# Performance work log

Measured on AMD Instinct MI355X. Metric: run time of the kernel, lower is better.

Reference implementation:

```python
import jax, jax.numpy as jnp
import numpy as np

NBINS = (128, 64, 32)
N_REGIONS = 5000
N_REGIONS_OI = 500
N_POINTS = 262144
SUM_H = sum(NBINS)            # 224
SUM_W = sum(n - 1 for n in NBINS)  # 221


def _spline_level(x, uw_region, uh_pt, local_ix):
    """One quadratic-spline level.
    x: [N] inputs in [0,1); uw_region: [R, n-1] region unnormalized widths;
    uh_pt: [N, n] per-point unnormalized heights (embedding + delta);
    local_ix: [N] int mapping points -> rows of uw_region.
    """
    # region-level widths / bin locations (calculate_widths / calculate_bin_locations)
    widths = jax.nn.softmax(uw_region, axis=-1)                # [R, n-1]
    bl = jnp.cumsum(widths, axis=-1)
    bl = bl.at[:, -1].set(1.0)
    bin_locations = jnp.pad(bl, ((0, 0), (1, 0)))              # [R, n]

    # gather per point (index_select(0, local_region_ix))
    widths_pt = widths[local_ix]                               # [N, n-1]
    bin_loc_pt = bin_locations[local_ix]                       # [N, n]

    # calculate_heights: exp then normalize so trapezoid integral == 1
    he = jnp.exp(uh_pt)                                        # [N, n]
    area = jnp.sum(0.5 * (he[:, :-1] + he[:, 1:]) * widths_pt, axis=-1, keepdims=True)
    heights = he / area                                        # [N, n]

    # calculate_bin_left_cdf
    cdf = jnp.cumsum(0.5 * (heights[:, :-1] + heights[:, 1:]) * widths_pt, axis=-1)
    cdf = cdf.at[:, -1].set(1.0)
    bin_left_cdf = jnp.pad(cdf, ((0, 0), (1, 0)))              # [N, n]

    # searchsorted(bin_locations, x, side='left') - 1, clamped to valid bins
    n = bin_loc_pt.shape[-1]
    bin_idx = jnp.clip(jnp.sum(bin_loc_pt < x[:, None], axis=-1) - 1, 0, n - 2)  # [N]

    take = lambda a, i: jnp.take_along_axis(a, i[:, None], axis=-1)[:, 0]
    in_loc = take(bin_loc_pt, bin_idx)
    in_w = take(widths_pt, bin_idx)
    in_cdf = take(bin_left_cdf, bin_idx)
    h_l = take(heights, bin_idx)
    h_r = take(heights, bin_idx + 1)

    alpha = (x - in_loc) / in_w
    a = 0.5 * (h_r - h_l) * in_w
    b = h_l * in_w
    out = a * alpha * alpha + b * alpha + in_cdf
    logabsdet = jnp.log(alpha * (h_r - h_l) + h_l)
    return out, logabsdet


def setup_inputs() -> dict:
    key = jax.random.key(0)
    k1, k2, k3, k4, k5, k6 = jax.random.split(key, 6)
    x = jax.random.uniform(k1, (N_POINTS,), dtype=jnp.float32)
    regions_oi = jax.random.randint(k2, (N_REGIONS_OI,), 0, N_REGIONS, dtype=jnp.int32)
    local_region_ix = jax.random.randint(k3, (N_POINTS,), 0, N_REGIONS_OI, dtype=jnp.int32)
    delta = jax.random.normal(k4, (N_POINTS, SUM_H), dtype=jnp.float32)
    # learned sparse embedding tables (init to random for a nontrivial baseline)
    heights_emb = 0.1 * jax.random.normal(k5, (N_REGIONS, SUM_H), dtype=jnp.float32)
    widths_emb = 0.1 * jax.random.normal(k6, (N_REGIONS, SUM_W), dtype=jnp.float32)
    return {"x": x, "regions_oi": regions_oi, "local_region_ix": local_region_ix,
            "delta": delta, "heights_emb": heights_emb, "widths_emb": widths_emb}


def reference(x, regions_oi, local_region_ix, delta, heights_emb, widths_emb):
    uh_all = heights_emb[regions_oi]   # [R, 224]
    uw_all = widths_emb[regions_oi]    # [R, 221]
    out = x
    logdet = jnp.zeros_like(x)
    oh = 0
    ow = 0
    for n in NBINS:
        uw = uw_all[:, ow:ow + (n - 1)]                               # [R, n-1]
        uh_pt = uh_all[local_region_ix][:, oh:oh + n] + delta[:, oh:oh + n]  # [N, n]
        out, ld = _spline_level(out, uw, uh_pt, local_region_ix)
        logdet = logdet + ld
        oh += n
        ow += n - 1
    return out, logdet
```

## Files before the change

kernel.cpp:

```cpp
#include <hip/hip_runtime.h>

#define NPOINTS 262144
#define SUMH 224
#define SUMW 221
#define NREG 500

__device__ __forceinline__ float rlane(float v, int l) {
  return __int_as_float(__builtin_amdgcn_readlane(__float_as_int(v), l));
}
template<int CTRL>
__device__ __forceinline__ float dpp_add(float x) {
  return x + __int_as_float(__builtin_amdgcn_update_dpp(0, __float_as_int(x), CTRL, 0xF, 0xF, false));
}
template<int CTRL>
__device__ __forceinline__ float dpp_max(float x) {
  return fmaxf(x, __int_as_float(__builtin_amdgcn_update_dpp(__float_as_int(x), __float_as_int(x), CTRL, 0xF, 0xF, false)));
}
__device__ __forceinline__ float wave_sum(float x) {
  x = dpp_add<0x111>(x); x = dpp_add<0x112>(x); x = dpp_add<0x114>(x);
  x = dpp_add<0x118>(x); x = dpp_add<0x142>(x); x = dpp_add<0x143>(x);
  return rlane(x, 63);
}
__device__ __forceinline__ float wave_max(float x) {
  x = dpp_max<0x111>(x); x = dpp_max<0x112>(x); x = dpp_max<0x114>(x);
  x = dpp_max<0x118>(x); x = dpp_max<0x142>(x); x = dpp_max<0x143>(x);
  return rlane(x, 63);
}

__device__ __forceinline__ float grp_sum(float x) {
  x += __int_as_float(__builtin_amdgcn_update_dpp(0, __float_as_int(x), 0xB1,  0xF, 0xF, true));
  x += __int_as_float(__builtin_amdgcn_update_dpp(0, __float_as_int(x), 0x4E,  0xF, 0xF, true));
  x += __int_as_float(__builtin_amdgcn_update_dpp(0, __float_as_int(x), 0x141, 0xF, 0xF, true));
  x += __int_as_float(__builtin_amdgcn_update_dpp(0, __float_as_int(x), 0x140, 0xF, 0xF, true));
  return x;
}
__device__ __forceinline__ int grp_sum_i(int x) {
  x += __builtin_amdgcn_update_dpp(0, x, 0xB1,  0xF, 0xF, true);
  x += __builtin_amdgcn_update_dpp(0, x, 0x4E,  0xF, 0xF, true);
  x += __builtin_amdgcn_update_dpp(0, x, 0x141, 0xF, 0xF, true);
  x += __builtin_amdgcn_update_dpp(0, x, 0x140, 0xF, 0xF, true);
  return x;
}


template<int M, int SRC, int DST, int NB>
__device__ __forceinline__ void region_level(const float* __restrict__ wrow,
    float* __restrict__ BL, float* __restrict__ HW, float* __restrict__ HM,
    int lane, float* lds)
{
  float v0 = (lane < M) ? wrow[SRC + lane] : -1e30f;
  float v1 = -1e30f;
  if constexpr (NB == 128) { if (lane + 64 < M) v1 = wrow[SRC + lane + 64]; }
  float m = wave_max(fmaxf(v0, v1));
  float e0 = __expf(v0 - m);
  float e1 = (NB == 128) ? __expf(v1 - m) : 0.0f;
  float s = wave_sum(e0 + e1);
  float inv = 1.0f / s;
  if (lane < NB) lds[lane] = e0;
  if constexpr (NB == 128) lds[lane + 64] = e1;
  __syncthreads();
  if (lane < NB) {
    HW[DST + lane] = 0.5f * e0 * inv;
    HM[DST + lane] = (lane == 0) ? 0.0f : 0.5f * lds[lane - 1] * inv;
  }
  if constexpr (NB == 128) {
    HW[DST + lane + 64] = 0.5f * e1 * inv;
    HM[DST + lane + 64] = 0.5f * lds[lane + 63] * inv;
  }
  if (lane == 0) {
    BL[DST] = 0.0f;
    float run = 0.0f;
    for (int k = 0; k < M; ++k) {
      run += lds[k];
      BL[DST + 1 + k] = (k == M - 1) ? 1.0f : run * inv;
    }
  }
  __syncthreads();
}

__global__ void __launch_bounds__(64) region_kernel(
    const int* __restrict__ roi, const float* __restrict__ wemb,
    float* __restrict__ wsBL, float* __restrict__ wsHW, float* __restrict__ wsHM)
{
  __shared__ float lds[128];
  int rix = blockIdx.x;
  int lane = threadIdx.x;
  int greg = roi[rix];
  const float* wrow = wemb + (size_t)greg * SUMW;
  float* BL = wsBL + (size_t)rix * SUMH;
  float* HW = wsHW + (size_t)rix * SUMH;
  float* HM = wsHM + (size_t)rix * SUMH;
  region_level<127,   0,   0, 128>(wrow, BL, HW, HM, lane, lds);
  region_level< 63, 127, 128,  64>(wrow, BL, HW, HM, lane, lds);
  region_level< 31, 190, 192,  32>(wrow, BL, HW, HM, lane, lds);
}


template<int NB, int OFF, int C>
__device__ __forceinline__ void level(float& xv, float& logdet,
    const float* __restrict__ U, const float* __restrict__ D,
    const float* __restrict__ BLt, const float* __restrict__ HWt,
    const float* __restrict__ HMt, int s)
{
  float u[C], d[C], bl[C], hw[C], hm[C];
  if constexpr (C >= 4) {
#pragma unroll
    for (int v = 0; v < C / 4; ++v) {
      int c0 = OFF + (s * (C / 4) + v) * 4;
      float4 a = *(const float4*)(U   + c0);
      float4 b = *(const float4*)(D   + c0);
      float4 e = *(const float4*)(BLt + c0);
      float4 f = *(const float4*)(HWt + c0);
      float4 g = *(const float4*)(HMt + c0);
      u[4*v+0]=a.x; u[4*v+1]=a.y; u[4*v+2]=a.z; u[4*v+3]=a.w;
      d[4*v+0]=b.x; d[4*v+1]=b.y; d[4*v+2]=b.z; d[4*v+3]=b.w;
      bl[4*v+0]=e.x; bl[4*v+1]=e.y; bl[4*v+2]=e.z; bl[4*v+3]=e.w;
      hw[4*v+0]=f.x; hw[4*v+1]=f.y; hw[4*v+2]=f.z; hw[4*v+3]=f.w;
      hm[4*v+0]=g.x; hm[4*v+1]=g.y; hm[4*v+2]=g.z; hm[4*v+3]=g.w;
    }
  } else {
    int c0 = OFF + s * 2;
    float2 a = *(const float2*)(U   + c0);
    float2 b = *(const float2*)(D   + c0);
    float2 e = *(const float2*)(BLt + c0);
    float2 f = *(const float2*)(HWt + c0);
    float2 g = *(const float2*)(HMt + c0);
    u[0]=a.x; u[1]=a.y; d[0]=b.x; d[1]=b.y; bl[0]=e.x; bl[1]=e.y;
    hw[0]=f.x; hw[1]=f.y; hm[0]=g.x; hm[1]=g.y;
  }

  int cnt = 0;
  float he[C];
#pragma unroll
  for (int i = 0; i < C; ++i) {
    he[i] = __expf(u[i] + d[i]);
    cnt += (bl[i] < xv) ? 1 : 0;
  }
  cnt = grp_sum_i(cnt);
  int bi = min(max(cnt - 1, 0), NB - 2);

  float area = 0.0f, pr = 0.0f;
#pragma unroll
  for (int i = 0; i < C; ++i) {
    float t = he[i] * (hw[i] + hm[i]);
    area += t;
    int j = s * C + i;
    pr += (j <= bi) ? t : 0.0f;
  }
  area = grp_sum(area);
  pr   = grp_sum(pr);

  float inloc = BLt[OFF + bi];
  float hwbi  = HWt[OFF + bi];
  float hl = __expf(U[OFF + bi]     + D[OFF + bi]);
  float hr = __expf(U[OFF + bi + 1] + D[OFF + bi + 1]);

  float part = pr - hl * hwbi;
  float inw = 2.0f * hwbi;
  float inv_area = __builtin_amdgcn_rcpf(area);
  float alpha = (xv - inloc) * __builtin_amdgcn_rcpf(inw);
  float dh = hr - hl;
  float outv = ((0.5f * dh * alpha + hl) * alpha * inw + part) * inv_area;
  logdet += (__log2f(alpha * dh + hl) - __log2f(area)) * 0.69314718055994531f;
  xv = outv;
}

__global__ void __launch_bounds__(256) spline_kernel(
    const float* __restrict__ x, const int* __restrict__ roi,
    const int* __restrict__ lix, const float* __restrict__ delta,
    const float* __restrict__ hemb,
    const float* __restrict__ wsBL, const float* __restrict__ wsHW,
    const float* __restrict__ wsHM, float* __restrict__ out)
{
  int tid  = (int)(blockIdx.x * blockDim.x + threadIdx.x);
  int wid  = tid >> 6;
  int lane = (int)(threadIdx.x & 63);
  int grp  = lane >> 4;
  int s    = lane & 15;
  int pid  = wid * 4 + grp;
  if (pid >= NPOINTS) return;

  float xv = x[pid];
  int r    = lix[pid];
  int greg = roi[r];
  const float* U   = hemb  + (size_t)greg * SUMH;
  const float* D   = delta + (size_t)pid  * SUMH;
  const float* BLt = wsBL  + (size_t)r    * SUMH;
  const float* HWt = wsHW  + (size_t)r    * SUMH;
  const float* HMt = wsHM  + (size_t)r    * SUMH;

  float logdet = 0.0f;
  level<128,   0, 8>(xv, logdet, U, D, BLt, HWt, HMt, s);
  level< 64, 128, 4>(xv, logdet, U, D, BLt, HWt, HMt, s);
  level< 32, 192, 2>(xv, logdet, U, D, BLt, HWt, HMt, s);

  if (s == 0) {
    out[pid] = xv;
    out[NPOINTS + pid] = logdet;
  }
}


extern "C" void kernel_launch(void* const* d_in, const int* in_sizes, int n_in,
                              void* d_out, int out_size, void* d_ws, size_t ws_size,
                              hipStream_t stream) {
  const float* x     = (const float*)d_in[0];
  const int*   roi   = (const int*)  d_in[1];
  const int*   lix   = (const int*)  d_in[2];
  const float* delta = (const float*)d_in[3];
  const float* hemb  = (const float*)d_in[4];
  const float* wemb  = (const float*)d_in[5];

  float* wsBL = (float*)d_ws;
  float* wsHW = wsBL + (size_t)NREG * SUMH;
  float* wsHM = wsHW + (size_t)NREG * SUMH;

  region_kernel<<<NREG, 64, 0, stream>>>(roi, wemb, wsBL, wsHW, wsHM);
  spline_kernel<<<NPOINTS / 16, 256, 0, stream>>>(x, roi, lix, delta, hemb,
                                                  wsBL, wsHW, wsHM, (float*)d_out);
}
```

Before: 389.0 us.

## Precompute per-level prefix sums and fetch bin values via lane permutes

Splits each spline level into an x-independent prep phase (load, exp, prefix scan of trapezoid areas, log/reciprocal of area) and an x-dependent apply phase. All three levels' loads and scans are issued up front, so memory latency overlaps instead of being serialized by the x dependency chain. The scattered global re-reads of the selected bin's values are replaced with register selects plus ds_bpermute across the 16-lane group. This costs more live registers (three levels' arrays held at once), which may reduce occupancy. The early-return bounds check is also removed.

```diff
diff --git a/kernel.cpp b/kernel.cpp
--- a/kernel.cpp
+++ b/kernel.cpp
@@ -40,6 +40,23 @@
   x += __builtin_amdgcn_update_dpp(0, x, 0x141, 0xF, 0xF, true);
   x += __builtin_amdgcn_update_dpp(0, x, 0x140, 0xF, 0xF, true);
   return x;
+}
+__device__ __forceinline__ float row_scan_incl(float x) {
+  x += __int_as_float(__builtin_amdgcn_update_dpp(0, __float_as_int(x), 0x111, 0xF, 0xF, true));
+  x += __int_as_float(__builtin_amdgcn_update_dpp(0, __float_as_int(x), 0x112, 0xF, 0xF, true));
+  x += __int_as_float(__builtin_amdgcn_update_dpp(0, __float_as_int(x), 0x114, 0xF, 0xF, true));
+  x += __int_as_float(__builtin_amdgcn_update_dpp(0, __float_as_int(x), 0x118, 0xF, 0xF, true));
+  return x;
+}
+__device__ __forceinline__ float bperm(int lane, float v) {
+  return __int_as_float(__builtin_amdgcn_ds_bpermute(lane << 2, __float_as_int(v)));
+}
+template<int C>
+__device__ __forceinline__ float sel(const float (&a)[C], int idx) {
+  float r = a[0];
+#pragma unroll
+  for (int i = 1; i < C; ++i) r = (idx == i) ? a[i] : r;
+  return r;
 }
 
 
@@ -96,74 +113,84 @@
 }
 
 
-template<int NB, int OFF, int C>
-__device__ __forceinline__ void level(float& xv, float& logdet,
-    const float* __restrict__ U, const float* __restrict__ D,
-    const float* __restrict__ BLt, const float* __restrict__ HWt,
-    const float* __restrict__ HMt, int s)
-{
-  float u[C], d[C], bl[C], hw[C], hm[C];
-  if constexpr (C >= 4) {
-#pragma unroll
-    for (int v = 0; v < C / 4; ++v) {
-      int c0 = OFF + (s * (C / 4) + v) * 4;
-      float4 a = *(const float4*)(U   + c0);
-      float4 b = *(const float4*)(D   + c0);
-      float4 e = *(const float4*)(BLt + c0);
-      float4 f = *(const float4*)(HWt + c0);
-      float4 g = *(const float4*)(HMt + c0);
-      u[4*v+0]=a.x; u[4*v+1]=a.y; u[4*v+2]=a.z; u[4*v+3]=a.w;
-      d[4*v+0]=b.x; d[4*v+1]=b.y; d[4*v+2]=b.z; d[4*v+3]=b.w;
-      bl[4*v+0]=e.x; bl[4*v+1]=e.y; bl[4*v+2]=e.z; bl[4*v+3]=e.w;
-      hw[4*v+0]=f.x; hw[4*v+1]=f.y; hw[4*v+2]=f.z; hw[4*v+3]=f.w;
-      hm[4*v+0]=g.x; hm[4*v+1]=g.y; hm[4*v+2]=g.z; hm[4*v+3]=g.w;
+template<int NB, int OFF, int C, int LOG2C>
+struct Level {
+  float he[C], bl[C], hw[C], Q[C];
+  float larea, invarea;
+
+  __device__ __forceinline__ void prep(const float* __restrict__ U,
+      const float* __restrict__ D, const float* __restrict__ BLt,
+      const float* __restrict__ HWt, const float* __restrict__ HMt, int s)
+  {
+    float t[C];
+    if constexpr (C >= 4) {
+#pragma unroll
+      for (int v = 0; v < C / 4; ++v) {
+        int c0 = OFF + (s * (C / 4) + v) * 4;
+        float4 a = *(const float4*)(U   + c0);
+        float4 b = *(const float4*)(D   + c0);
+        float4 e = *(const float4*)(BLt + c0);
+        float4 f = *(const float4*)(HWt + c0);
+        float4 g = *(const float4*)(HMt + c0);
+        he[4*v+0] = __expf(a.x + b.x); he[4*v+1] = __expf(a.y + b.y);
+        he[4*v+2] = __expf(a.z + b.z); he[4*v+3] = __expf(a.w + b.w);
+        bl[4*v+0]=e.x; bl[4*v+1]=e.y; bl[4*v+2]=e.z; bl[4*v+3]=e.w;
+        hw[4*v+0]=f.x; hw[4*v+1]=f.y; hw[4*v+2]=f.z; hw[4*v+3]=f.w;
+        t[4*v+0] = he[4*v+0]*(f.x+g.x); t[4*v+1] = he[4*v+1]*(f.y+g.y);
+        t[4*v+2] = he[4*v+2]*(f.z+g.z); t[4*v+3] = he[4*v+3]*(f.w+g.w);
+      }
+    } else {
+      int c0 = OFF + s * 2;
+      float2 a = *(const float2*)(U   + c0);
+      float2 b = *(const float2*)(D   + c0);
+      float2 e = *(const float2*)(BLt + c0);
+      float2 f = *(const float2*)(HWt + c0);
+      float2 g = *(const float2*)(HMt + c0);
+      he[0] = __expf(a.x + b.x); he[1] = __expf(a.y + b.y);
+      bl[0]=e.x; bl[1]=e.y; hw[0]=f.x; hw[1]=f.y;
+      t[0] = he[0]*(f.x+g.x); t[1] = he[1]*(f.y+g.y);
     }
-  } else {
-    int c0 = OFF + s * 2;
-    float2 a = *(const float2*)(U   + c0);
-    float2 b = *(const float2*)(D   + c0);
-    float2 e = *(const float2*)(BLt + c0);
-    float2 f = *(const float2*)(HWt + c0);
-    float2 g = *(const float2*)(HMt + c0);
-    u[0]=a.x; u[1]=a.y; d[0]=b.x; d[1]=b.y; bl[0]=e.x; bl[1]=e.y;
-    hw[0]=f.x; hw[1]=f.y; hm[0]=g.x; hm[1]=g.y;
-  }
-
-  int cnt = 0;
-  float he[C];
-#pragma unroll
-  for (int i = 0; i < C; ++i) {
-    he[i] = __expf(u[i] + d[i]);
-    cnt += (bl[i] < xv) ? 1 : 0;
-  }
-  cnt = grp_sum_i(cnt);
-  int bi = min(max(cnt - 1, 0), NB - 2);
-
-  float area = 0.0f, pr = 0.0f;
-#pragma unroll
-  for (int i = 0; i < C; ++i) {
-    float t = he[i] * (hw[i] + hm[i]);
-    area += t;
-    int j = s * C + i;
-    pr += (j <= bi) ? t : 0.0f;
-  }
-  area = grp_sum(area);
-  pr   = grp_sum(pr);
-
-  float inloc = BLt[OFF + bi];
-  float hwbi  = HWt[OFF + bi];
-  float hl = __expf(U[OFF + bi]     + D[OFF + bi]);
-  float hr = __expf(U[OFF + bi + 1] + D[OFF + bi + 1]);
-
-  float part = pr - hl * hwbi;
-  float inw = 2.0f * hwbi;
-  float inv_area = __builtin_amdgcn_rcpf(area);
-  float alpha = (xv - inloc) * __builtin_amdgcn_rcpf(inw);
-  float dh = hr - hl;
-  float outv = ((0.5f * dh * alpha + hl) * alpha * inw + part) * inv_area;
-  logdet += (__log2f(alpha * dh + hl) - __log2f(area)) * 0.69314718055994531f;
-  xv = outv;
-}
+    float p = 0.0f;
+#pragma unroll
+    for (int i = 0; i < C; ++i) { p += t[i]; Q[i] = p; }
+    float sc = row_scan_incl(p);
+    float excl = sc - p;
+#pragma unroll
+    for (int i = 0; i < C; ++i) Q[i] += excl;
+    float area = grp_sum(p);
+    larea = __log2f(area);
+    invarea = __builtin_amdgcn_rcpf(area);
+  }
+
+  __device__ __forceinline__ void apply(float& xv, float& logdet, int grp, int s) {
+    int cnt = 0;
+#pragma unroll
+    for (int i = 0; i < C; ++i) cnt += (bl[i] < xv) ? 1 : 0;
+    cnt = grp_sum_i(cnt);
+    int bi = min(max(cnt - 1, 0), NB - 2);
+    int sl0 = bi & (C - 1);
+    int ln0 = (grp << 4) + (bi >> LOG2C);
+    int bj = bi + 1;
+    int sl1 = bj & (C - 1);
+    int ln1 = (grp << 4) + (bj >> LOG2C);
+    float qs  = sel<C>(Q,  sl0);
+    float bls = sel<C>(bl, sl0);
+    float hws = sel<C>(hw, sl0);
+    float hes = sel<C>(he, sl0);
+    float he1 = sel<C>(he, sl1);
+    float q_b  = bperm(ln0, qs);
+    float bl_b = bperm(ln0, bls);
+    float hw_b = bperm(ln0, hws);
+    float hl   = bperm(ln0, hes);
+    float hr   = bperm(ln1, he1);
+    float part = q_b - hl * hw_b;
+    float inw = 2.0f * hw_b;
+    float alpha = (xv - bl_b) * __builtin_amdgcn_rcpf(inw);
+    float dh = hr - hl;
+    xv = ((0.5f * dh * alpha + hl) * alpha * inw + part) * invarea;
+    logdet += (__log2f(alpha * dh + hl) - larea) * 0.69314718055994531f;
+  }
+};
 
 __global__ void __launch_bounds__(256) spline_kernel(
     const float* __restrict__ x, const int* __restrict__ roi,
@@ -178,7 +205,6 @@
   int grp  = lane >> 4;
   int s    = lane & 15;
   int pid  = wid * 4 + grp;
-  if (pid >= NPOINTS) return;
 
   float xv = x[pid];
   int r    = lix[pid];
@@ -189,10 +215,16 @@
   const float* HWt = wsHW  + (size_t)r    * SUMH;
   const float* HMt = wsHM  + (size_t)r    * SUMH;
 
+  Level<128,   0, 8, 3> L0;
+  Level< 64, 128, 4, 2> L1;
+  Level< 32, 192, 2, 1> L2;
+  L0.prep(U, D, BLt, HWt, HMt, s);
+  L1.prep(U, D, BLt, HWt, HMt, s);
+  L2.prep(U, D, BLt, HWt, HMt, s);
   float logdet = 0.0f;
-  level<128,   0, 8>(xv, logdet, U, D, BLt, HWt, HMt, s);
-  level< 64, 128, 4>(xv, logdet, U, D, BLt, HWt, HMt, s);
-  level< 32, 192, 2>(xv, logdet, U, D, BLt, HWt, HMt, s);
+  L0.apply(xv, logdet, grp, s);
+  L1.apply(xv, logdet, grp, s);
+  L2.apply(xv, logdet, grp, s);
 
   if (s == 0) {
     out[pid] = xv;
```

Measured after the change: 502.9 us. +29.3%, slower.

## Precompute per-level areas ahead of bin search and replace gathers with masked group reductions

Applied to the files above, without the earlier changes.

The spline kernel now splits each level into a prep phase and an apply phase. Prep loads the data, exponentiates and reduces the area, and it does not depend on x, so levels 1 and 2 are prepped before the previous level is applied and their loads can overlap with its dependent chain. The apply phase finds the selected bin with a one-hot mask built from neighbour comparisons via DPP, then gets hl, hr, location and width through group sums, which removes the dependent scattered global loads and extra exp calls. The region kernel stores HW+HM premultiplied and computes the bin-location cumsum with a wave scan instead of a serial single-lane loop. The trade-off is more registers held across levels and five group reductions per level instead of two.

```diff
diff --git a/kernel.cpp b/kernel.cpp
--- a/kernel.cpp
+++ b/kernel.cpp
@@ -9,43 +9,45 @@
   return __int_as_float(__builtin_amdgcn_readlane(__float_as_int(v), l));
 }
 template<int CTRL>
-__device__ __forceinline__ float dpp_add(float x) {
-  return x + __int_as_float(__builtin_amdgcn_update_dpp(0, __float_as_int(x), CTRL, 0xF, 0xF, false));
+__device__ __forceinline__ float dpp0(float x) {
+  return __int_as_float(__builtin_amdgcn_update_dpp(0, __float_as_int(x), CTRL, 0xF, 0xF, true));
+}
+template<int CTRL, int RM>
+__device__ __forceinline__ float dpp_rm(float x) {
+  return __int_as_float(__builtin_amdgcn_update_dpp(0, __float_as_int(x), CTRL, RM, 0xF, false));
 }
 template<int CTRL>
-__device__ __forceinline__ float dpp_max(float x) {
+__device__ __forceinline__ float dpp_max_(float x) {
   return fmaxf(x, __int_as_float(__builtin_amdgcn_update_dpp(__float_as_int(x), __float_as_int(x), CTRL, 0xF, 0xF, false)));
 }
 __device__ __forceinline__ float wave_sum(float x) {
-  x = dpp_add<0x111>(x); x = dpp_add<0x112>(x); x = dpp_add<0x114>(x);
-  x = dpp_add<0x118>(x); x = dpp_add<0x142>(x); x = dpp_add<0x143>(x);
+  x += dpp0<0x111>(x); x += dpp0<0x112>(x); x += dpp0<0x114>(x); x += dpp0<0x118>(x);
+  x += dpp_rm<0x142, 0xA>(x); x += dpp_rm<0x143, 0xC>(x);
   return rlane(x, 63);
 }
 __device__ __forceinline__ float wave_max(float x) {
-  x = dpp_max<0x111>(x); x = dpp_max<0x112>(x); x = dpp_max<0x114>(x);
-  x = dpp_max<0x118>(x); x = dpp_max<0x142>(x); x = dpp_max<0x143>(x);
+  x = dpp_max_<0x111>(x); x = dpp_max_<0x112>(x); x = dpp_max_<0x114>(x);
+  x = dpp_max_<0x118>(x); x = dpp_max_<0x142>(x); x = dpp_max_<0x143>(x);
   return rlane(x, 63);
 }
-
+__device__ __forceinline__ float wave_scan_incl(float x) {
+  x += dpp0<0x111>(x); x += dpp0<0x112>(x); x += dpp0<0x114>(x); x += dpp0<0x118>(x);
+  x += dpp_rm<0x142, 0xA>(x);
+  x += dpp_rm<0x143, 0xC>(x);
+  return x;
+}
 __device__ __forceinline__ float grp_sum(float x) {
-  x += __int_as_float(__builtin_amdgcn_update_dpp(0, __float_as_int(x), 0xB1,  0xF, 0xF, true));
-  x += __int_as_float(__builtin_amdgcn_update_dpp(0, __float_as_int(x), 0x4E,  0xF, 0xF, true));
-  x += __int_as_float(__builtin_amdgcn_update_dpp(0, __float_as_int(x), 0x141, 0xF, 0xF, true));
-  x += __int_as_float(__builtin_amdgcn_update_dpp(0, __float_as_int(x), 0x140, 0xF, 0xF, true));
-  return x;
-}
-__device__ __forceinline__ int grp_sum_i(int x) {
-  x += __builtin_amdgcn_update_dpp(0, x, 0xB1,  0xF, 0xF, true);
-  x += __builtin_amdgcn_update_dpp(0, x, 0x4E,  0xF, 0xF, true);
-  x += __builtin_amdgcn_update_dpp(0, x, 0x141, 0xF, 0xF, true);
-  x += __builtin_amdgcn_update_dpp(0, x, 0x140, 0xF, 0xF, true);
+  x += dpp0<0xB1>(x);
+  x += dpp0<0x4E>(x);
+  x += dpp0<0x141>(x);
+  x += dpp0<0x140>(x);
   return x;
 }
 
 
 template<int M, int SRC, int DST, int NB>
 __device__ __forceinline__ void region_level(const float* __restrict__ wrow,
-    float* __restrict__ BL, float* __restrict__ HW, float* __restrict__ HM,
+    float* __restrict__ BL, float* __restrict__ HW, float* __restrict__ HS,
     int lane, float* lds)
 {
   float v0 = (lane < M) ? wrow[SRC + lane] : -1e30f;
@@ -61,26 +63,27 @@
   __syncthreads();
   if (lane < NB) {
     HW[DST + lane] = 0.5f * e0 * inv;
-    HM[DST + lane] = (lane == 0) ? 0.0f : 0.5f * lds[lane - 1] * inv;
+    float prev = (lane == 0) ? 0.0f : lds[lane - 1];
+    HS[DST + lane] = 0.5f * (e0 + prev) * inv;
   }
   if constexpr (NB == 128) {
     HW[DST + lane + 64] = 0.5f * e1 * inv;
-    HM[DST + lane + 64] = 0.5f * lds[lane + 63] * inv;
-  }
-  if (lane == 0) {
-    BL[DST] = 0.0f;
-    float run = 0.0f;
-    for (int k = 0; k < M; ++k) {
-      run += lds[k];
-      BL[DST + 1 + k] = (k == M - 1) ? 1.0f : run * inv;
-    }
+    HS[DST + lane + 64] = 0.5f * (e1 + lds[lane + 63]) * inv;
+  }
+  float incl0 = wave_scan_incl(e0);
+  if (lane == 0) BL[DST] = 0.0f;
+  if (lane < M) BL[DST + 1 + lane] = (lane == M - 1) ? 1.0f : incl0 * inv;
+  if constexpr (NB == 128) {
+    float incl1 = wave_scan_incl(e1) + rlane(incl0, 63);
+    int k = 64 + lane;
+    if (k < M) BL[DST + 1 + k] = (k == M - 1) ? 1.0f : incl1 * inv;
   }
   __syncthreads();
 }
 
 __global__ void __launch_bounds__(64) region_kernel(
     const int* __restrict__ roi, const float* __restrict__ wemb,
-    float* __restrict__ wsBL, float* __restrict__ wsHW, float* __restrict__ wsHM)
+    float* __restrict__ wsBL, float* __restrict__ wsHW, float* __restrict__ wsHS)
 {
   __shared__ float lds[128];
   int rix = blockIdx.x;
@@ -89,88 +92,97 @@
   const float* wrow = wemb + (size_t)greg * SUMW;
   float* BL = wsBL + (size_t)rix * SUMH;
   float* HW = wsHW + (size_t)rix * SUMH;
-  float* HM = wsHM + (size_t)rix * SUMH;
-  region_level<127,   0,   0, 128>(wrow, BL, HW, HM, lane, lds);
-  region_level< 63, 127, 128,  64>(wrow, BL, HW, HM, lane, lds);
-  region_level< 31, 190, 192,  32>(wrow, BL, HW, HM, lane, lds);
+  float* HS = wsHS + (size_t)rix * SUMH;
+  region_level<127,   0,   0, 128>(wrow, BL, HW, HS, lane, lds);
+  region_level< 63, 127, 128,  64>(wrow, BL, HW, HS, lane, lds);
+  region_level< 31, 190, 192,  32>(wrow, BL, HW, HS, lane, lds);
 }
 
 
 template<int NB, int OFF, int C>
-__device__ __forceinline__ void level(float& xv, float& logdet,
-    const float* __restrict__ U, const float* __restrict__ D,
-    const float* __restrict__ BLt, const float* __restrict__ HWt,
-    const float* __restrict__ HMt, int s)
-{
-  float u[C], d[C], bl[C], hw[C], hm[C];
-  if constexpr (C >= 4) {
-#pragma unroll
-    for (int v = 0; v < C / 4; ++v) {
-      int c0 = OFF + (s * (C / 4) + v) * 4;
-      float4 a = *(const float4*)(U   + c0);
-      float4 b = *(const float4*)(D   + c0);
-      float4 e = *(const float4*)(BLt + c0);
-      float4 f = *(const float4*)(HWt + c0);
-      float4 g = *(const float4*)(HMt + c0);
-      u[4*v+0]=a.x; u[4*v+1]=a.y; u[4*v+2]=a.z; u[4*v+3]=a.w;
-      d[4*v+0]=b.x; d[4*v+1]=b.y; d[4*v+2]=b.z; d[4*v+3]=b.w;
-      bl[4*v+0]=e.x; bl[4*v+1]=e.y; bl[4*v+2]=e.z; bl[4*v+3]=e.w;
-      hw[4*v+0]=f.x; hw[4*v+1]=f.y; hw[4*v+2]=f.z; hw[4*v+3]=f.w;
-      hm[4*v+0]=g.x; hm[4*v+1]=g.y; hm[4*v+2]=g.z; hm[4*v+3]=g.w;
+struct Lv {
+  float he[C], t[C], bl[C], hw[C];
+  float larea, invarea;
+
+  __device__ __forceinline__ void prep(const float* __restrict__ U,
+      const float* __restrict__ D, const float* __restrict__ BLt,
+      const float* __restrict__ HWt, const float* __restrict__ HSt, int s)
+  {
+    if constexpr (C >= 4) {
+#pragma unroll
+      for (int v = 0; v < C / 4; ++v) {
+        int c0 = OFF + (s * (C / 4) + v) * 4;
+        float4 a = *(const float4*)(U   + c0);
+        float4 b = *(const float4*)(D   + c0);
+        float4 e = *(const float4*)(BLt + c0);
+        float4 f = *(const float4*)(HWt + c0);
+        float4 g = *(const float4*)(HSt + c0);
+        he[4*v+0] = __expf(a.x + b.x); he[4*v+1] = __expf(a.y + b.y);
+        he[4*v+2] = __expf(a.z + b.z); he[4*v+3] = __expf(a.w + b.w);
+        t[4*v+0] = he[4*v+0] * g.x; t[4*v+1] = he[4*v+1] * g.y;
+        t[4*v+2] = he[4*v+2] * g.z; t[4*v+3] = he[4*v+3] * g.w;
+        bl[4*v+0]=e.x; bl[4*v+1]=e.y; bl[4*v+2]=e.z; bl[4*v+3]=e.w;
+        hw[4*v+0]=f.x; hw[4*v+1]=f.y; hw[4*v+2]=f.z; hw[4*v+3]=f.w;
+      }
+    } else {
+      int c0 = OFF + s * 2;
+      float2 a = *(const float2*)(U   + c0);
+      float2 b = *(const float2*)(D   + c0);
+      float2 e = *(const float2*)(BLt + c0);
+      float2 f = *(const float2*)(HWt + c0);
+      float2 g = *(const float2*)(HSt + c0);
+      he[0] = __expf(a.x + b.x); he[1] = __expf(a.y + b.y);
+      t[0] = he[0] * g.x; t[1] = he[1] * g.y;
+      bl[0]=e.x; bl[1]=e.y; hw[0]=f.x; hw[1]=f.y;
     }
-  } else {
-    int c0 = OFF + s * 2;
-    float2 a = *(const float2*)(U   + c0);
-    float2 b = *(const float2*)(D   + c0);
-    float2 e = *(const float2*)(BLt + c0);
-    float2 f = *(const float2*)(HWt + c0);
-    float2 g = *(const float2*)(HMt + c0);
-    u[0]=a.x; u[1]=a.y; d[0]=b.x; d[1]=b.y; bl[0]=e.x; bl[1]=e.y;
-    hw[0]=f.x; hw[1]=f.y; hm[0]=g.x; hm[1]=g.y;
-  }
-
-  int cnt = 0;
-  float he[C];
-#pragma unroll
-  for (int i = 0; i < C; ++i) {
-    he[i] = __expf(u[i] + d[i]);
-    cnt += (bl[i] < xv) ? 1 : 0;
-  }
-  cnt = grp_sum_i(cnt);
-  int bi = min(max(cnt - 1, 0), NB - 2);
-
-  float area = 0.0f, pr = 0.0f;
-#pragma unroll
-  for (int i = 0; i < C; ++i) {
-    float t = he[i] * (hw[i] + hm[i]);
-    area += t;
-    int j = s * C + i;
-    pr += (j <= bi) ? t : 0.0f;
-  }
-  area = grp_sum(area);
-  pr   = grp_sum(pr);
-
-  float inloc = BLt[OFF + bi];
-  float hwbi  = HWt[OFF + bi];
-  float hl = __expf(U[OFF + bi]     + D[OFF + bi]);
-  float hr = __expf(U[OFF + bi + 1] + D[OFF + bi + 1]);
-
-  float part = pr - hl * hwbi;
-  float inw = 2.0f * hwbi;
-  float inv_area = __builtin_amdgcn_rcpf(area);
-  float alpha = (xv - inloc) * __builtin_amdgcn_rcpf(inw);
-  float dh = hr - hl;
-  float outv = ((0.5f * dh * alpha + hl) * alpha * inw + part) * inv_area;
-  logdet += (__log2f(alpha * dh + hl) - __log2f(area)) * 0.69314718055994531f;
-  xv = outv;
-}
+    float asum = 0.0f;
+#pragma unroll
+    for (int i = 0; i < C; ++i) asum += t[i];
+    float area = grp_sum(asum);
+    larea = __log2f(area);
+    invarea = __builtin_amdgcn_rcpf(area);
+  }
+
+  __device__ __forceinline__ void apply(float& xv, float& logdet, int s) {
+    float f[C];
+#pragma unroll
+    for (int i = 0; i < C; ++i) f[i] = (bl[i] < xv) ? 1.0f : 0.0f;
+    if (s == 0)  f[0]     = 1.0f;
+    if (s == 15) f[C - 1] = 0.0f;
+    float fN  = dpp0<0x101>(f[0]);
+    float heN = dpp0<0x101>(he[0]);
+    float hl = 0.0f, hr = 0.0f, loc = 0.0f, hwm = 0.0f, pt = 0.0f;
+#pragma unroll
+    for (int i = 0; i < C; ++i) {
+      float fnext  = (i < C - 1) ? f[i + 1]  : fN;
+      float henext = (i < C - 1) ? he[i + 1] : heN;
+      float mi = f[i] * (1.0f - fnext);
+      hl  += he[i] * mi;
+      hr  += henext * mi;
+      loc += bl[i] * mi;
+      hwm += hw[i] * mi;
+      pt  += t[i] * f[i];
+    }
+    hl  = grp_sum(hl);
+    hr  = grp_sum(hr);
+    loc = grp_sum(loc);
+    hwm = grp_sum(hwm);
+    pt  = grp_sum(pt);
+    float part = pt - hl * hwm;
+    float inw = 2.0f * hwm;
+    float alpha = (xv - loc) * __builtin_amdgcn_rcpf(inw);
+    float dh = hr - hl;
+    xv = ((0.5f * dh * alpha + hl) * alpha * inw + part) * invarea;
+    logdet += (__log2f(alpha * dh + hl) - larea) * 0.69314718055994531f;
+  }
+};
 
 __global__ void __launch_bounds__(256) spline_kernel(
     const float* __restrict__ x, const int* __restrict__ roi,
     const int* __restrict__ lix, const float* __restrict__ delta,
     const float* __restrict__ hemb,
     const float* __restrict__ wsBL, const float* __restrict__ wsHW,
-    const float* __restrict__ wsHM, float* __restrict__ out)
+    const float* __restrict__ wsHS, float* __restrict__ out)
 {
   int tid  = (int)(blockIdx.x * blockDim.x + threadIdx.x);
   int wid  = tid >> 6;
@@ -178,7 +190,6 @@
   int grp  = lane >> 4;
   int s    = lane & 15;
   int pid  = wid * 4 + grp;
-  if (pid >= NPOINTS) return;
 
   float xv = x[pid];
   int r    = lix[pid];
@@ -187,12 +198,18 @@
   const float* D   = delta + (size_t)pid  * SUMH;
   const float* BLt = wsBL  + (size_t)r    * SUMH;
   const float* HWt = wsHW  + (size_t)r    * SUMH;
-  const float* HMt = wsHM  + (size_t)r    * SUMH;
-
+  const float* HSt = wsHS  + (size_t)r    * SUMH;
+
+  Lv<128,   0, 8> L0;
+  Lv< 64, 128, 4> L1;
+  Lv< 32, 192, 2> L2;
   float logdet = 0.0f;
-  level<128,   0, 8>(xv, logdet, U, D, BLt, HWt, HMt, s);
-  level< 64, 128, 4>(xv, logdet, U, D, BLt, HWt, HMt, s);
-  level< 32, 192, 2>(xv, logdet, U, D, BLt, HWt, HMt, s);
+  L0.prep(U, D, BLt, HWt, HSt, s);
+  L1.prep(U, D, BLt, HWt, HSt, s);
+  L0.apply(xv, logdet, s);
+  L2.prep(U, D, BLt, HWt, HSt, s);
+  L1.apply(xv, logdet, s);
+  L2.apply(xv, logdet, s);
 
   if (s == 0) {
     out[pid] = xv;
@@ -213,9 +230,9 @@
 
   float* wsBL = (float*)d_ws;
   float* wsHW = wsBL + (size_t)NREG * SUMH;
-  float* wsHM = wsHW + (size_t)NREG * SUMH;
-
-  region_kernel<<<NREG, 64, 0, stream>>>(roi, wemb, wsBL, wsHW, wsHM);
+  float* wsHS = wsHW + (size_t)NREG * SUMH;
+
+  region_kernel<<<NREG, 64, 0, stream>>>(roi, wemb, wsBL, wsHW, wsHS);
   spline_kernel<<<NPOINTS / 16, 256, 0, stream>>>(x, roi, lix, delta, hemb,
-                                                  wsBL, wsHW, wsHM, (float*)d_out);
-}
+                                                  wsBL, wsHW, wsHS, (float*)d_out);
+}
```

Result: faster. 358.7 us (-7.8%).
